# Performance work log

Measured on AMD Instinct MI355X. Metric: run time of the kernel, lower is better.

## Reference

```python
import jax, jax.numpy as jnp
import numpy as np

LEAKY_ALPHA = 0.2  # TF default for tf.nn.leaky_relu


def setup_inputs() -> dict:
    key = jax.random.key(0)
    ks = jax.random.split(key, 5)
    B, N, F, O, H = 2, 4096, 256, 64, 4
    x = jax.random.normal(ks[0], (B, N, F), dtype=jnp.float32)
    bias = jax.random.normal(ks[1], (B, N, N), dtype=jnp.float32)
    W = jax.random.normal(ks[2], (H, F, O), dtype=jnp.float32) * (1.0 / np.sqrt(F))
    a = jax.random.normal(ks[3], (H, O), dtype=jnp.float32) * (1.0 / np.sqrt(O))
    b = jax.random.normal(ks[4], (H, O), dtype=jnp.float32) * 0.01
    return {"x": x, "bias": bias, "W": W, "a": a, "b": b}


def reference(x, bias, W, a, b):
    # x: [B,N,F], bias: [B,N,N], W: [H,F,O], a: [H,O], b: [H,O]
    h = jnp.einsum('bnf,hfo->bhno', x, W)          # transformed inputs per head
    w = jnp.einsum('bhno,ho->bhn', h, a)           # scalar score per node
    scores = w[:, :, :, None] + w[:, :, None, :]   # [B,H,N,N]: w_i + w_j
    logits = jax.nn.leaky_relu(scores, LEAKY_ALPHA) + bias[:, None, :, :]
    coefs = jax.nn.softmax(logits, axis=3)
    heads = jnp.einsum('bhnm,bhmo->bhno', coefs, h) + b[None, :, None, :]
    return jnp.mean(heads, axis=1)                 # (1/H) * sum of heads -> [B,N,O]
```

## Files before the change

kernel.cpp:

```cpp
#include <hip/hip_runtime.h>
#include <hip/hip_bf16.h>


constexpr int Bc = 2, Nc = 4096, Fc = 256, Oc = 64, Hc = 4;
constexpr float ALPHA = 0.2f;
constexpr float LOG2E = 1.4426950408889634f;

constexpr int BSTR = 260;
constexpr int BBUF = 16 * BSTR;
constexpr int SLOTF = 1088;
constexpr int SMEMF = 8 * SLOTF;

typedef __attribute__((ext_vector_type(8))) short bf16x8;
typedef __attribute__((ext_vector_type(4))) float f32x4;

static __device__ inline short f2bf(float x) {
    __hip_bfloat16 h = __float2bfloat16(x);
    return *reinterpret_cast<short*>(&h);
}

static __device__ inline int frag_off(int jt, int k, int lane, int t) {
    return jt * 4096 + k * 512 + lane * 8 + t;
}

__global__ __launch_bounds__(256) void k_h(const float* __restrict__ x,
                                           const float* __restrict__ W,
                                           const float* __restrict__ a,
                                           short* __restrict__ hTB,
                                           float* __restrict__ wout) {
    __shared__ float xs[64][132];
    const int nb = Nc / 64;
    const int blk = blockIdx.x;
    const int nt = blk % nb;
    const int bh = blk / nb;
    const int h = bh % Hc;
    const int b = bh / Hc;
    const int tid = threadIdx.x;
    const int o_id = tid & 15, n_id = tid >> 4;
    const int o0 = o_id * 4, n0 = n_id * 4;

    float acc[4][4] = {};

    for (int fs = 0; fs < Fc; fs += 128) {
#pragma unroll
        for (int it = 0; it < 8; ++it) {
            int idx = it * 256 + tid;
            int r = idx >> 5, c = idx & 31;
            const float4 v = *reinterpret_cast<const float4*>(
                &x[((size_t)(b * Nc + nt * 64 + r)) * Fc + fs + c * 4]);
            *reinterpret_cast<float4*>(&xs[r][c * 4]) = v;
        }
        __syncthreads();
        for (int f = 0; f < 128; ++f) {
            const float4 wv = *reinterpret_cast<const float4*>(
                &W[((size_t)(h * Fc + fs + f)) * Oc + o0]);
            float xv[4];
#pragma unroll
            for (int r = 0; r < 4; ++r) xv[r] = xs[n0 + r][f];
#pragma unroll
            for (int r = 0; r < 4; ++r) {
                acc[r][0] = __builtin_fmaf(xv[r], wv.x, acc[r][0]);
                acc[r][1] = __builtin_fmaf(xv[r], wv.y, acc[r][1]);
                acc[r][2] = __builtin_fmaf(xv[r], wv.z, acc[r][2]);
                acc[r][3] = __builtin_fmaf(xv[r], wv.w, acc[r][3]);
            }
        }
        __syncthreads();
    }

    const float4 av = *reinterpret_cast<const float4*>(&a[h * Oc + o0]);
    float part[4];
#pragma unroll
    for (int r = 0; r < 4; ++r) {
        part[r] = acc[r][0] * av.x + acc[r][1] * av.y + acc[r][2] * av.z +
                  acc[r][3] * av.w;
#pragma unroll
        for (int off = 1; off < 16; off <<= 1)
            part[r] += __shfl_xor(part[r], off, 64);
    }
    const int n_glob = nt * 64 + n0;
    if (o_id == 0) {
#pragma unroll
        for (int r = 0; r < 4; ++r)
            wout[((size_t)(b * Hc + h)) * Nc + n_glob + r] = part[r];
    }
    const int sub = n0 >> 5;
    const int lg = (n0 >> 3) & 3;
    const int t0 = n0 & 7;
    short* base = hTB + ((size_t)(b * Hc + h)) * (Nc * Oc);
#pragma unroll
    for (int c = 0; c < 4; ++c) {
        const int o = o0 + c;
        const int of = o >> 4, li = o & 15;
        short4 v;
        v.x = f2bf(acc[0][c]);
        v.y = f2bf(acc[1][c]);
        v.z = f2bf(acc[2][c]);
        v.w = f2bf(acc[3][c]);
        *reinterpret_cast<short4*>(&base[frag_off(nt, of * 2 + sub, lg * 16 + li, t0)]) = v;
    }
}

__global__ __launch_bounds__(1024, 4) void k_attn(
    const float* __restrict__ bias, const float* __restrict__ bvec,
    const float* __restrict__ wrow, const short* __restrict__ hTB,
    float* __restrict__ out) {
    __shared__ float smem[SMEMF];

    const int blk = blockIdx.x;
    const int b = blk / (Nc / 16);
    const int i0 = (blk % (Nc / 16)) * 16;
    const int tid = threadIdx.x;
    const int w = tid >> 6;
    const int hd = w & 3;
    const int q = w >> 2;
    const int lane = tid & 63;
    const int li = lane & 15, lg = lane >> 4;
    const int jl0 = lg * 8;

    const float wi = wrow[((size_t)(b * Hc + hd)) * Nc + i0 + li];
    const float* __restrict__ wj_base = &wrow[((size_t)(b * Hc + hd)) * Nc];
    const short* __restrict__ fb =
        hTB + ((size_t)(b * Hc + hd)) * (Nc * Oc) + lane * 8;

    const int srow = tid >> 6, scol4 = tid & 63;
    const float* __restrict__ stage_src =
        &bias[((size_t)(b * Nc + i0 + srow)) * Nc + scol4 * 4];
    float* const stage_dst0 = &smem[srow * BSTR + scol4 * 4];

    f32x4 acc[4] = {{0.f, 0.f, 0.f, 0.f},
                    {0.f, 0.f, 0.f, 0.f},
                    {0.f, 0.f, 0.f, 0.f},
                    {0.f, 0.f, 0.f, 0.f}};
    float l_run = 0.f;

    {
        const float4 p0 = *reinterpret_cast<const float4*>(stage_src);
        *reinterpret_cast<float4*>(stage_dst0) = p0;
    }
    float4 preA = *reinterpret_cast<const float4*>(stage_src + 256);
    float4 preB = *reinterpret_cast<const float4*>(stage_src + 512);
    float4 preC = preB;
    __syncthreads();

#pragma unroll 1
    for (int st = 0; st < 16; ++st) {
        if (st + 1 < 16)
            *reinterpret_cast<float4*>(stage_dst0 + ((st + 1) & 1) * BBUF) = preA;
        if (st + 3 < 16)
            preC = *reinterpret_cast<const float4*>(stage_src + (size_t)(st + 3) * 256);

        const int jt = st * 4 + q;
        bf16x8 fr[8];
#pragma unroll
        for (int k = 0; k < 8; ++k)
            fr[k] = *reinterpret_cast<const bf16x8*>(fb + jt * 4096 + k * 512);
        const float* bp = &smem[(st & 1) * BBUF + li * BSTR + q * 64 + jl0];
        const float4 b03 = *reinterpret_cast<const float4*>(bp);
        const float4 b47 = *reinterpret_cast<const float4*>(bp + 4);
        const float4 b8b = *reinterpret_cast<const float4*>(bp + 32);
        const float4 bcf = *reinterpret_cast<const float4*>(bp + 36);
        float s[16] = {b03.x, b03.y, b03.z, b03.w, b47.x, b47.y, b47.z, b47.w,
                       b8b.x, b8b.y, b8b.z, b8b.w, bcf.x, bcf.y, bcf.z, bcf.w};
        const int j0 = st * 256 + q * 64;
#pragma unroll
        for (int u = 0; u < 4; ++u) {
            const float4 wv = *reinterpret_cast<const float4*>(
                &wj_base[j0 + (u >> 1) * 32 + jl0 + (u & 1) * 4]);
            float v;
            v = wi + wv.x; s[u * 4 + 0] += fmaxf(v, ALPHA * v);
            v = wi + wv.y; s[u * 4 + 1] += fmaxf(v, ALPHA * v);
            v = wi + wv.z; s[u * 4 + 2] += fmaxf(v, ALPHA * v);
            v = wi + wv.w; s[u * 4 + 3] += fmaxf(v, ALPHA * v);
        }
        float tsum = 0.f;
#pragma unroll
        for (int t = 0; t < 16; ++t) {
            s[t] = __builtin_amdgcn_exp2f(s[t] * LOG2E);
            tsum += s[t];
        }
        l_run += tsum;
        bf16x8 pa[2];
#pragma unroll
        for (int sub = 0; sub < 2; ++sub)
#pragma unroll
            for (int t = 0; t < 8; ++t) pa[sub][t] = f2bf(s[sub * 8 + t]);
        __builtin_amdgcn_s_setprio(1);
#pragma unroll
        for (int of = 0; of < 4; ++of) {
            acc[of] = __builtin_amdgcn_mfma_f32_16x16x32_bf16(pa[0], fr[of * 2 + 0],
                                                              acc[of], 0, 0, 0);
            acc[of] = __builtin_amdgcn_mfma_f32_16x16x32_bf16(pa[1], fr[of * 2 + 1],
                                                              acc[of], 0, 0, 0);
        }
        __builtin_amdgcn_s_setprio(0);
        __syncthreads();
        preA = preB;
        preB = preC;
    }

    auto write_state = [&](int s) {
        float* base = smem + s * SLOTF;
#pragma unroll
        for (int of = 0; of < 4; ++of)
            *reinterpret_cast<f32x4*>(&base[of * 256 + lane * 4]) = acc[of];
        base[1024 + lane] = l_run;
    };
    auto merge_state = [&](int s) {
        float* base = smem + s * SLOTF;
#pragma unroll
        for (int of = 0; of < 4; ++of) {
            const f32x4 p = *reinterpret_cast<const f32x4*>(&base[of * 256 + lane * 4]);
            acc[of][0] += p[0];
            acc[of][1] += p[1];
            acc[of][2] += p[2];
            acc[of][3] += p[3];
        }
        l_run += base[1024 + lane];
    };

    if (q & 1) write_state((q >> 1) * 4 + hd);
    __syncthreads();
    if (!(q & 1)) merge_state((q >> 1) * 4 + hd);
    __syncthreads();
    if (q == 2) write_state(hd);
    __syncthreads();
    if (q == 0) merge_state(hd);
    __syncthreads();
    if (q == 0) {
        float lrow = l_run + __shfl_xor(l_run, 16, 64);
        lrow += __shfl_xor(lrow, 32, 64);
        const float linv = 1.0f / lrow;
        float lr[4];
#pragma unroll
        for (int r = 0; r < 4; ++r) lr[r] = __shfl(linv, lg * 4 + r, 64);
#pragma unroll
        for (int of = 0; of < 4; ++of)
#pragma unroll
            for (int r = 0; r < 4; ++r) acc[of][r] *= lr[r];
        write_state(hd);
    }
    __syncthreads();
    const int row = tid >> 6, col = tid & 63;
    const int ofo = col >> 4, lio = col & 15, lgo = row >> 2, ro = row & 3;
    const int eoff = ofo * 256 + (lgo * 16 + lio) * 4 + ro;
    float osum = 0.f;
#pragma unroll
    for (int h = 0; h < 4; ++h) osum += smem[h * SLOTF + eoff];
    const float bm = 0.25f * (bvec[col] + bvec[Oc + col] + bvec[2 * Oc + col] +
                              bvec[3 * Oc + col]);
    out[((size_t)(b * Nc + i0 + row)) * Oc + col] = 0.25f * osum + bm;
}

extern "C" void kernel_launch(void* const* d_in, const int* in_sizes, int n_in,
                              void* d_out, int out_size, void* d_ws, size_t ws_size,
                              hipStream_t stream) {
    const float* x = (const float*)d_in[0];
    const float* bias = (const float*)d_in[1];
    const float* W = (const float*)d_in[2];
    const float* a = (const float*)d_in[3];
    const float* bvec = (const float*)d_in[4];
    float* out = (float*)d_out;

    short* hTB = (short*)d_ws;
    float* wbuf = (float*)((char*)d_ws + (size_t)Bc * Hc * Oc * Nc * 2);

    k_h<<<Bc * Hc * (Nc / 64), 256, 0, stream>>>(x, W, a, hTB, wbuf);
    k_attn<<<Bc * (Nc / 16), 1024, 0, stream>>>(bias, bvec, wbuf, hTB, out);
}
```

Measured before the change: 104.1 us.

## Process 32 query rows per attention block to reuse h fragments

Each attention block now handles 32 rows instead of 16, so every bf16 h fragment loaded from global memory feeds two sets of MFMAs (two row tiles). Grid size is halved, and the bias staging buffer doubles to hold 32 rows. Bias prefetch depth drops from three stages to two. The intent is to halve global traffic for h, which is re-read by every row block, at the cost of more registers (double accumulators), larger shared memory, and fewer blocks for occupancy.

```diff
diff --git a/kernel.cpp b/kernel.cpp
--- a/kernel.cpp
+++ b/kernel.cpp
@@ -7,9 +7,9 @@
 constexpr float LOG2E = 1.4426950408889634f;
 
 constexpr int BSTR = 260;
-constexpr int BBUF = 16 * BSTR;
+constexpr int BBUF = 32 * BSTR;
+constexpr int SMEMF = 2 * BBUF;
 constexpr int SLOTF = 1088;
-constexpr int SMEMF = 8 * SLOTF;
 
 typedef __attribute__((ext_vector_type(8))) short bf16x8;
 typedef __attribute__((ext_vector_type(4))) float f32x4;
@@ -108,8 +108,8 @@
     __shared__ float smem[SMEMF];
 
     const int blk = blockIdx.x;
-    const int b = blk / (Nc / 16);
-    const int i0 = (blk % (Nc / 16)) * 16;
+    const int b = blk / (Nc / 32);
+    const int i0 = (blk % (Nc / 32)) * 32;
     const int tid = threadIdx.x;
     const int w = tid >> 6;
     const int hd = w & 3;
@@ -118,138 +118,165 @@
     const int li = lane & 15, lg = lane >> 4;
     const int jl0 = lg * 8;
 
-    const float wi = wrow[((size_t)(b * Hc + hd)) * Nc + i0 + li];
+    const float wi0 = wrow[((size_t)(b * Hc + hd)) * Nc + i0 + li];
+    const float wi1 = wrow[((size_t)(b * Hc + hd)) * Nc + i0 + 16 + li];
     const float* __restrict__ wj_base = &wrow[((size_t)(b * Hc + hd)) * Nc];
     const short* __restrict__ fb =
         hTB + ((size_t)(b * Hc + hd)) * (Nc * Oc) + lane * 8;
 
     const int srow = tid >> 6, scol4 = tid & 63;
-    const float* __restrict__ stage_src =
+    const float* __restrict__ ssrc0 =
         &bias[((size_t)(b * Nc + i0 + srow)) * Nc + scol4 * 4];
-    float* const stage_dst0 = &smem[srow * BSTR + scol4 * 4];
-
-    f32x4 acc[4] = {{0.f, 0.f, 0.f, 0.f},
-                    {0.f, 0.f, 0.f, 0.f},
-                    {0.f, 0.f, 0.f, 0.f},
-                    {0.f, 0.f, 0.f, 0.f}};
-    float l_run = 0.f;
-
-    {
-        const float4 p0 = *reinterpret_cast<const float4*>(stage_src);
-        *reinterpret_cast<float4*>(stage_dst0) = p0;
-    }
-    float4 preA = *reinterpret_cast<const float4*>(stage_src + 256);
-    float4 preB = *reinterpret_cast<const float4*>(stage_src + 512);
-    float4 preC = preB;
+    const float* __restrict__ ssrc1 = ssrc0 + (size_t)16 * Nc;
+    float* const sdst0 = &smem[srow * BSTR + scol4 * 4];
+    float* const sdst1 = sdst0 + 16 * BSTR;
+
+    f32x4 acc[2][4] = {{{0.f, 0.f, 0.f, 0.f}, {0.f, 0.f, 0.f, 0.f},
+                        {0.f, 0.f, 0.f, 0.f}, {0.f, 0.f, 0.f, 0.f}},
+                       {{0.f, 0.f, 0.f, 0.f}, {0.f, 0.f, 0.f, 0.f},
+                        {0.f, 0.f, 0.f, 0.f}, {0.f, 0.f, 0.f, 0.f}}};
+    float l0 = 0.f, l1 = 0.f;
+
+    *reinterpret_cast<float4*>(sdst0) = *reinterpret_cast<const float4*>(ssrc0);
+    *reinterpret_cast<float4*>(sdst1) = *reinterpret_cast<const float4*>(ssrc1);
+    float4 preA0 = *reinterpret_cast<const float4*>(ssrc0 + 256);
+    float4 preA1 = *reinterpret_cast<const float4*>(ssrc1 + 256);
+    float4 preB0 = preA0, preB1 = preA1;
     __syncthreads();
 
 #pragma unroll 1
     for (int st = 0; st < 16; ++st) {
-        if (st + 1 < 16)
-            *reinterpret_cast<float4*>(stage_dst0 + ((st + 1) & 1) * BBUF) = preA;
-        if (st + 3 < 16)
-            preC = *reinterpret_cast<const float4*>(stage_src + (size_t)(st + 3) * 256);
+        if (st + 1 < 16) {
+            float* d = sdst0 + ((st + 1) & 1) * BBUF;
+            *reinterpret_cast<float4*>(d) = preA0;
+            *reinterpret_cast<float4*>(d + 16 * BSTR) = preA1;
+        }
+        if (st + 2 < 16) {
+            preB0 = *reinterpret_cast<const float4*>(ssrc0 + (size_t)(st + 2) * 256);
+            preB1 = *reinterpret_cast<const float4*>(ssrc1 + (size_t)(st + 2) * 256);
+        }
 
         const int jt = st * 4 + q;
         bf16x8 fr[8];
 #pragma unroll
         for (int k = 0; k < 8; ++k)
             fr[k] = *reinterpret_cast<const bf16x8*>(fb + jt * 4096 + k * 512);
-        const float* bp = &smem[(st & 1) * BBUF + li * BSTR + q * 64 + jl0];
-        const float4 b03 = *reinterpret_cast<const float4*>(bp);
-        const float4 b47 = *reinterpret_cast<const float4*>(bp + 4);
-        const float4 b8b = *reinterpret_cast<const float4*>(bp + 32);
-        const float4 bcf = *reinterpret_cast<const float4*>(bp + 36);
-        float s[16] = {b03.x, b03.y, b03.z, b03.w, b47.x, b47.y, b47.z, b47.w,
-                       b8b.x, b8b.y, b8b.z, b8b.w, bcf.x, bcf.y, bcf.z, bcf.w};
         const int j0 = st * 256 + q * 64;
+        float4 wv[4];
+#pragma unroll
+        for (int u = 0; u < 4; ++u)
+            wv[u] = *reinterpret_cast<const float4*>(
+                &wj_base[j0 + (u >> 1) * 32 + jl0 + (u & 1) * 4]);
+        float lk[16];
 #pragma unroll
         for (int u = 0; u < 4; ++u) {
-            const float4 wv = *reinterpret_cast<const float4*>(
-                &wj_base[j0 + (u >> 1) * 32 + jl0 + (u & 1) * 4]);
-            float v;
-            v = wi + wv.x; s[u * 4 + 0] += fmaxf(v, ALPHA * v);
-            v = wi + wv.y; s[u * 4 + 1] += fmaxf(v, ALPHA * v);
-            v = wi + wv.z; s[u * 4 + 2] += fmaxf(v, ALPHA * v);
-            v = wi + wv.w; s[u * 4 + 3] += fmaxf(v, ALPHA * v);
-        }
-        float tsum = 0.f;
-#pragma unroll
-        for (int t = 0; t < 16; ++t) {
-            s[t] = __builtin_amdgcn_exp2f(s[t] * LOG2E);
-            tsum += s[t];
-        }
-        l_run += tsum;
-        bf16x8 pa[2];
-#pragma unroll
-        for (int sub = 0; sub < 2; ++sub)
-#pragma unroll
-            for (int t = 0; t < 8; ++t) pa[sub][t] = f2bf(s[sub * 8 + t]);
+            lk[u * 4 + 0] = wv[u].x;
+            lk[u * 4 + 1] = wv[u].y;
+            lk[u * 4 + 2] = wv[u].z;
+            lk[u * 4 + 3] = wv[u].w;
+        }
+
+        bf16x8 pa[2][2];
+#pragma unroll
+        for (int t = 0; t < 2; ++t) {
+            const float wi = t ? wi1 : wi0;
+            const float* bp =
+                &smem[(st & 1) * BBUF + (t * 16 + li) * BSTR + q * 64 + jl0];
+            const float4 b03 = *reinterpret_cast<const float4*>(bp);
+            const float4 b47 = *reinterpret_cast<const float4*>(bp + 4);
+            const float4 b8b = *reinterpret_cast<const float4*>(bp + 32);
+            const float4 bcf = *reinterpret_cast<const float4*>(bp + 36);
+            float s[16] = {b03.x, b03.y, b03.z, b03.w, b47.x, b47.y, b47.z,
+                           b47.w, b8b.x, b8b.y, b8b.z, b8b.w, bcf.x, bcf.y,
+                           bcf.z, bcf.w};
+            float tsum = 0.f;
+#pragma unroll
+            for (int k = 0; k < 16; ++k) {
+                const float v = wi + lk[k];
+                s[k] += fmaxf(v, ALPHA * v);
+                s[k] = __builtin_amdgcn_exp2f(s[k] * LOG2E);
+                tsum += s[k];
+            }
+            if (t) l1 += tsum; else l0 += tsum;
+#pragma unroll
+            for (int sub = 0; sub < 2; ++sub)
+#pragma unroll
+                for (int k = 0; k < 8; ++k) pa[t][sub][k] = f2bf(s[sub * 8 + k]);
+        }
         __builtin_amdgcn_s_setprio(1);
 #pragma unroll
-        for (int of = 0; of < 4; ++of) {
-            acc[of] = __builtin_amdgcn_mfma_f32_16x16x32_bf16(pa[0], fr[of * 2 + 0],
-                                                              acc[of], 0, 0, 0);
-            acc[of] = __builtin_amdgcn_mfma_f32_16x16x32_bf16(pa[1], fr[of * 2 + 1],
-                                                              acc[of], 0, 0, 0);
-        }
+        for (int t = 0; t < 2; ++t)
+#pragma unroll
+            for (int of = 0; of < 4; ++of) {
+                acc[t][of] = __builtin_amdgcn_mfma_f32_16x16x32_bf16(
+                    pa[t][0], fr[of * 2 + 0], acc[t][of], 0, 0, 0);
+                acc[t][of] = __builtin_amdgcn_mfma_f32_16x16x32_bf16(
+                    pa[t][1], fr[of * 2 + 1], acc[t][of], 0, 0, 0);
+            }
         __builtin_amdgcn_s_setprio(0);
         __syncthreads();
-        preA = preB;
-        preB = preC;
-    }
-
-    auto write_state = [&](int s) {
-        float* base = smem + s * SLOTF;
-#pragma unroll
-        for (int of = 0; of < 4; ++of)
-            *reinterpret_cast<f32x4*>(&base[of * 256 + lane * 4]) = acc[of];
-        base[1024 + lane] = l_run;
-    };
-    auto merge_state = [&](int s) {
-        float* base = smem + s * SLOTF;
-#pragma unroll
-        for (int of = 0; of < 4; ++of) {
-            const f32x4 p = *reinterpret_cast<const f32x4*>(&base[of * 256 + lane * 4]);
-            acc[of][0] += p[0];
-            acc[of][1] += p[1];
-            acc[of][2] += p[2];
-            acc[of][3] += p[3];
-        }
-        l_run += base[1024 + lane];
-    };
-
-    if (q & 1) write_state((q >> 1) * 4 + hd);
-    __syncthreads();
-    if (!(q & 1)) merge_state((q >> 1) * 4 + hd);
-    __syncthreads();
-    if (q == 2) write_state(hd);
-    __syncthreads();
-    if (q == 0) merge_state(hd);
-    __syncthreads();
-    if (q == 0) {
-        float lrow = l_run + __shfl_xor(l_run, 16, 64);
-        lrow += __shfl_xor(lrow, 32, 64);
-        const float linv = 1.0f / lrow;
-        float lr[4];
-#pragma unroll
-        for (int r = 0; r < 4; ++r) lr[r] = __shfl(linv, lg * 4 + r, 64);
-#pragma unroll
-        for (int of = 0; of < 4; ++of)
-#pragma unroll
-            for (int r = 0; r < 4; ++r) acc[of][r] *= lr[r];
-        write_state(hd);
-    }
-    __syncthreads();
+        preA0 = preB0;
+        preA1 = preB1;
+    }
+
     const int row = tid >> 6, col = tid & 63;
     const int ofo = col >> 4, lio = col & 15, lgo = row >> 2, ro = row & 3;
     const int eoff = ofo * 256 + (lgo * 16 + lio) * 4 + ro;
-    float osum = 0.f;
-#pragma unroll
-    for (int h = 0; h < 4; ++h) osum += smem[h * SLOTF + eoff];
     const float bm = 0.25f * (bvec[col] + bvec[Oc + col] + bvec[2 * Oc + col] +
                               bvec[3 * Oc + col]);
-    out[((size_t)(b * Nc + i0 + row)) * Oc + col] = 0.25f * osum + bm;
+
+#pragma unroll 1
+    for (int t = 0; t < 2; ++t) {
+        float lr_ = t ? l1 : l0;
+        auto write_state = [&](int s) {
+            float* base = smem + s * SLOTF;
+#pragma unroll
+            for (int of = 0; of < 4; ++of)
+                *reinterpret_cast<f32x4*>(&base[of * 256 + lane * 4]) = acc[t][of];
+            base[1024 + lane] = lr_;
+        };
+        auto merge_state = [&](int s) {
+            float* base = smem + s * SLOTF;
+#pragma unroll
+            for (int of = 0; of < 4; ++of) {
+                const f32x4 p =
+                    *reinterpret_cast<const f32x4*>(&base[of * 256 + lane * 4]);
+                acc[t][of][0] += p[0];
+                acc[t][of][1] += p[1];
+                acc[t][of][2] += p[2];
+                acc[t][of][3] += p[3];
+            }
+            lr_ += base[1024 + lane];
+        };
+
+        if (q & 1) write_state((q >> 1) * 4 + hd);
+        __syncthreads();
+        if (!(q & 1)) merge_state((q >> 1) * 4 + hd);
+        __syncthreads();
+        if (q == 2) write_state(hd);
+        __syncthreads();
+        if (q == 0) merge_state(hd);
+        __syncthreads();
+        if (q == 0) {
+            float lrow = lr_ + __shfl_xor(lr_, 16, 64);
+            lrow += __shfl_xor(lrow, 32, 64);
+            const float linv = 1.0f / lrow;
+            float sc[4];
+#pragma unroll
+            for (int r = 0; r < 4; ++r) sc[r] = __shfl(linv, lg * 4 + r, 64);
+#pragma unroll
+            for (int of = 0; of < 4; ++of)
+#pragma unroll
+                for (int r = 0; r < 4; ++r) acc[t][of][r] *= sc[r];
+            write_state(hd);
+        }
+        __syncthreads();
+        float osum = 0.f;
+#pragma unroll
+        for (int h = 0; h < 4; ++h) osum += smem[h * SLOTF + eoff];
+        out[((size_t)(b * Nc + i0 + t * 16 + row)) * Oc + col] = 0.25f * osum + bm;
+        __syncthreads();
+    }
 }
 
 extern "C" void kernel_launch(void* const* d_in, const int* in_sizes, int n_in,
@@ -266,5 +293,5 @@
     float* wbuf = (float*)((char*)d_ws + (size_t)Bc * Hc * Oc * Nc * 2);
 
     k_h<<<Bc * Hc * (Nc / 64), 256, 0, stream>>>(x, W, a, hTB, wbuf);
-    k_attn<<<Bc * (Nc / 16), 1024, 0, stream>>>(bias, bvec, wbuf, hTB, out);
-}
+    k_attn<<<Bc * (Nc / 32), 1024, 0, stream>>>(bias, bvec, wbuf, hTB, out);
+}
```

Result: slower. 215.5 us (+107.1%).

## Split attention per head into separate blocks and reduce heads in a new kernel

Applied to the files above, without the earlier changes.

The attention kernel now launches one 256-thread block per (batch, row tile, head) instead of one 1024-thread block covering all four heads. Each block writes normalized per-head outputs to a workspace buffer, and a new k_out kernel averages the heads and adds the mean bias. The bias staging drops its double buffering and register prefetch in favor of a synchronous load per step. The cost is that each bias tile is now fetched by four separate blocks, plus an extra global round trip and kernel launch. Load latency is also less hidden.

```diff
diff --git a/kernel.cpp b/kernel.cpp
--- a/kernel.cpp
+++ b/kernel.cpp
@@ -7,9 +7,8 @@
 constexpr float LOG2E = 1.4426950408889634f;
 
 constexpr int BSTR = 260;
-constexpr int BBUF = 16 * BSTR;
 constexpr int SLOTF = 1088;
-constexpr int SMEMF = 8 * SLOTF;
+constexpr int SMEMF = 16 * BSTR;
 
 typedef __attribute__((ext_vector_type(8))) short bf16x8;
 typedef __attribute__((ext_vector_type(4))) float f32x4;
@@ -101,32 +100,31 @@
     }
 }
 
-__global__ __launch_bounds__(1024, 4) void k_attn(
-    const float* __restrict__ bias, const float* __restrict__ bvec,
-    const float* __restrict__ wrow, const short* __restrict__ hTB,
-    float* __restrict__ out) {
+__global__ __launch_bounds__(256, 4) void k_attn(
+    const float* __restrict__ bias, const float* __restrict__ wrow,
+    const short* __restrict__ hTB, float* __restrict__ hps) {
     __shared__ float smem[SMEMF];
 
     const int blk = blockIdx.x;
-    const int b = blk / (Nc / 16);
-    const int i0 = (blk % (Nc / 16)) * 16;
+    const int hd = blk & 3;
+    const int it = (blk >> 2) & 255;
+    const int b = blk >> 10;
+    const int i0 = it * 16;
     const int tid = threadIdx.x;
-    const int w = tid >> 6;
-    const int hd = w & 3;
-    const int q = w >> 2;
+    const int q = tid >> 6;
     const int lane = tid & 63;
     const int li = lane & 15, lg = lane >> 4;
     const int jl0 = lg * 8;
 
     const float wi = wrow[((size_t)(b * Hc + hd)) * Nc + i0 + li];
-    const float* __restrict__ wj_base = &wrow[((size_t)(b * Hc + hd)) * Nc];
+    const float* __restrict__ wjb = &wrow[((size_t)(b * Hc + hd)) * Nc];
     const short* __restrict__ fb =
         hTB + ((size_t)(b * Hc + hd)) * (Nc * Oc) + lane * 8;
 
-    const int srow = tid >> 6, scol4 = tid & 63;
-    const float* __restrict__ stage_src =
-        &bias[((size_t)(b * Nc + i0 + srow)) * Nc + scol4 * 4];
-    float* const stage_dst0 = &smem[srow * BSTR + scol4 * 4];
+    const int srow = tid >> 4, scol = (tid & 15) * 4;
+    const float* __restrict__ ssrc =
+        &bias[((size_t)(b * Nc + i0 + srow)) * Nc + scol];
+    float* const sdst = &smem[srow * BSTR + scol];
 
     f32x4 acc[4] = {{0.f, 0.f, 0.f, 0.f},
                     {0.f, 0.f, 0.f, 0.f},
@@ -134,28 +132,25 @@
                     {0.f, 0.f, 0.f, 0.f}};
     float l_run = 0.f;
 
-    {
-        const float4 p0 = *reinterpret_cast<const float4*>(stage_src);
-        *reinterpret_cast<float4*>(stage_dst0) = p0;
-    }
-    float4 preA = *reinterpret_cast<const float4*>(stage_src + 256);
-    float4 preB = *reinterpret_cast<const float4*>(stage_src + 512);
-    float4 preC = preB;
-    __syncthreads();
-
 #pragma unroll 1
     for (int st = 0; st < 16; ++st) {
-        if (st + 1 < 16)
-            *reinterpret_cast<float4*>(stage_dst0 + ((st + 1) & 1) * BBUF) = preA;
-        if (st + 3 < 16)
-            preC = *reinterpret_cast<const float4*>(stage_src + (size_t)(st + 3) * 256);
+        const float* sp = ssrc + (size_t)st * 256;
+        const float4 t0 = *reinterpret_cast<const float4*>(sp);
+        const float4 t1 = *reinterpret_cast<const float4*>(sp + 64);
+        const float4 t2 = *reinterpret_cast<const float4*>(sp + 128);
+        const float4 t3 = *reinterpret_cast<const float4*>(sp + 192);
+        *reinterpret_cast<float4*>(sdst) = t0;
+        *reinterpret_cast<float4*>(sdst + 64) = t1;
+        *reinterpret_cast<float4*>(sdst + 128) = t2;
+        *reinterpret_cast<float4*>(sdst + 192) = t3;
+        __syncthreads();
 
         const int jt = st * 4 + q;
         bf16x8 fr[8];
 #pragma unroll
         for (int k = 0; k < 8; ++k)
             fr[k] = *reinterpret_cast<const bf16x8*>(fb + jt * 4096 + k * 512);
-        const float* bp = &smem[(st & 1) * BBUF + li * BSTR + q * 64 + jl0];
+        const float* bp = &smem[li * BSTR + q * 64 + jl0];
         const float4 b03 = *reinterpret_cast<const float4*>(bp);
         const float4 b47 = *reinterpret_cast<const float4*>(bp + 4);
         const float4 b8b = *reinterpret_cast<const float4*>(bp + 32);
@@ -166,7 +161,7 @@
 #pragma unroll
         for (int u = 0; u < 4; ++u) {
             const float4 wv = *reinterpret_cast<const float4*>(
-                &wj_base[j0 + (u >> 1) * 32 + jl0 + (u & 1) * 4]);
+                &wjb[j0 + (u >> 1) * 32 + jl0 + (u & 1) * 4]);
             float v;
             v = wi + wv.x; s[u * 4 + 0] += fmaxf(v, ALPHA * v);
             v = wi + wv.y; s[u * 4 + 1] += fmaxf(v, ALPHA * v);
@@ -175,81 +170,80 @@
         }
         float tsum = 0.f;
 #pragma unroll
-        for (int t = 0; t < 16; ++t) {
-            s[t] = __builtin_amdgcn_exp2f(s[t] * LOG2E);
-            tsum += s[t];
+        for (int k = 0; k < 16; ++k) {
+            s[k] = __builtin_amdgcn_exp2f(s[k] * LOG2E);
+            tsum += s[k];
         }
         l_run += tsum;
-        bf16x8 pa[2];
-#pragma unroll
-        for (int sub = 0; sub < 2; ++sub)
-#pragma unroll
-            for (int t = 0; t < 8; ++t) pa[sub][t] = f2bf(s[sub * 8 + t]);
+        bf16x8 pa0, pa1;
+#pragma unroll
+        for (int k = 0; k < 8; ++k) pa0[k] = f2bf(s[k]);
+#pragma unroll
+        for (int k = 0; k < 8; ++k) pa1[k] = f2bf(s[8 + k]);
         __builtin_amdgcn_s_setprio(1);
 #pragma unroll
         for (int of = 0; of < 4; ++of) {
-            acc[of] = __builtin_amdgcn_mfma_f32_16x16x32_bf16(pa[0], fr[of * 2 + 0],
+            acc[of] = __builtin_amdgcn_mfma_f32_16x16x32_bf16(pa0, fr[of * 2 + 0],
                                                               acc[of], 0, 0, 0);
-            acc[of] = __builtin_amdgcn_mfma_f32_16x16x32_bf16(pa[1], fr[of * 2 + 1],
+            acc[of] = __builtin_amdgcn_mfma_f32_16x16x32_bf16(pa1, fr[of * 2 + 1],
                                                               acc[of], 0, 0, 0);
         }
         __builtin_amdgcn_s_setprio(0);
         __syncthreads();
-        preA = preB;
-        preB = preC;
-    }
-
-    auto write_state = [&](int s) {
-        float* base = smem + s * SLOTF;
+    }
+
+    if (q) {
+        float* base = smem + (q - 1) * SLOTF;
 #pragma unroll
         for (int of = 0; of < 4; ++of)
             *reinterpret_cast<f32x4*>(&base[of * 256 + lane * 4]) = acc[of];
         base[1024 + lane] = l_run;
-    };
-    auto merge_state = [&](int s) {
-        float* base = smem + s * SLOTF;
-#pragma unroll
-        for (int of = 0; of < 4; ++of) {
-            const f32x4 p = *reinterpret_cast<const f32x4*>(&base[of * 256 + lane * 4]);
-            acc[of][0] += p[0];
-            acc[of][1] += p[1];
-            acc[of][2] += p[2];
-            acc[of][3] += p[3];
-        }
-        l_run += base[1024 + lane];
-    };
-
-    if (q & 1) write_state((q >> 1) * 4 + hd);
-    __syncthreads();
-    if (!(q & 1)) merge_state((q >> 1) * 4 + hd);
-    __syncthreads();
-    if (q == 2) write_state(hd);
-    __syncthreads();
-    if (q == 0) merge_state(hd);
+    }
     __syncthreads();
     if (q == 0) {
+#pragma unroll
+        for (int s = 0; s < 3; ++s) {
+            const float* base = smem + s * SLOTF;
+#pragma unroll
+            for (int of = 0; of < 4; ++of) {
+                const f32x4 p =
+                    *reinterpret_cast<const f32x4*>(&base[of * 256 + lane * 4]);
+                acc[of][0] += p[0];
+                acc[of][1] += p[1];
+                acc[of][2] += p[2];
+                acc[of][3] += p[3];
+            }
+            l_run += base[1024 + lane];
+        }
         float lrow = l_run + __shfl_xor(l_run, 16, 64);
         lrow += __shfl_xor(lrow, 32, 64);
         const float linv = 1.0f / lrow;
-        float lr[4];
-#pragma unroll
-        for (int r = 0; r < 4; ++r) lr[r] = __shfl(linv, lg * 4 + r, 64);
+        float sc[4];
+#pragma unroll
+        for (int r = 0; r < 4; ++r) sc[r] = __shfl(linv, lg * 4 + r, 64);
+        float* hp = hps + (((size_t)(b * Hc + hd)) * Nc + i0) * Oc;
 #pragma unroll
         for (int of = 0; of < 4; ++of)
 #pragma unroll
-            for (int r = 0; r < 4; ++r) acc[of][r] *= lr[r];
-        write_state(hd);
-    }
-    __syncthreads();
-    const int row = tid >> 6, col = tid & 63;
-    const int ofo = col >> 4, lio = col & 15, lgo = row >> 2, ro = row & 3;
-    const int eoff = ofo * 256 + (lgo * 16 + lio) * 4 + ro;
-    float osum = 0.f;
-#pragma unroll
-    for (int h = 0; h < 4; ++h) osum += smem[h * SLOTF + eoff];
+            for (int r = 0; r < 4; ++r)
+                hp[(size_t)(lg * 4 + r) * Oc + of * 16 + li] = acc[of][r] * sc[r];
+    }
+}
+
+__global__ __launch_bounds__(256) void k_out(const float* __restrict__ hps,
+                                             const float* __restrict__ bvec,
+                                             float* __restrict__ out) {
+    const int e = blockIdx.x * 256 + threadIdx.x;
+    const int col = e & 63;
+    const int bn = e >> 6;
+    const int b = bn >> 12;
+    const size_t plane = (size_t)Nc * Oc;
+    const size_t off = ((size_t)(b * Hc) * Nc + (bn & 4095)) * Oc + col;
+    const float v = hps[off] + hps[off + plane] + hps[off + 2 * plane] +
+                    hps[off + 3 * plane];
     const float bm = 0.25f * (bvec[col] + bvec[Oc + col] + bvec[2 * Oc + col] +
                               bvec[3 * Oc + col]);
-    out[((size_t)(b * Nc + i0 + row)) * Oc + col] = 0.25f * osum + bm;
+    out[e] = 0.25f * v + bm;
 }
 
 extern "C" void kernel_launch(void* const* d_in, const int* in_sizes, int n_in,
@@ -262,9 +256,13 @@
     const float* bvec = (const float*)d_in[4];
     float* out = (float*)d_out;
 
-    short* hTB = (short*)d_ws;
-    float* wbuf = (float*)((char*)d_ws + (size_t)Bc * Hc * Oc * Nc * 2);
+    char* ws = (char*)d_ws;
+    short* hTB = (short*)ws;
+    float* wbuf = (float*)(ws + (size_t)Bc * Hc * Oc * Nc * 2);
+    float* hps = (float*)(ws + (size_t)Bc * Hc * Oc * Nc * 2 +
+                          (size_t)Bc * Hc * Nc * 4);
 
     k_h<<<Bc * Hc * (Nc / 64), 256, 0, stream>>>(x, W, a, hTB, wbuf);
-    k_attn<<<Bc * (Nc / 16), 1024, 0, stream>>>(bias, bvec, wbuf, hTB, out);
-}
+    k_attn<<<Bc * (Nc / 16) * Hc, 256, 0, stream>>>(bias, wbuf, hTB, hps);
+    k_out<<<(Bc * Nc * Oc) / 256, 256, 0, stream>>>(hps, bvec, out);
+}
```

New measurement: 133.6 us. 28.3% more time.
